# Kernel tuning notes

Hardware: AMD Instinct MI355X
Metric: run time of the kernel (lower is better)

The kernel has to match this reference:

```python
import jax, jax.numpy as jnp
import numpy as np

B, T, N = 512, 1024, 50
ROOT_IDX, END_IDX = 0, 1
NEG_INF = -10000.0


def setup_inputs() -> dict:
    key = jax.random.key(0)
    k1, k2, k3, k4 = jax.random.split(key, 4)
    input_features = jax.random.normal(k1, (B, T, N), dtype=jnp.float32)
    # xavier_uniform on [N, N]: bound = sqrt(6 / (N + N))
    bound = float(np.sqrt(6.0 / (N + N)))
    log_transitions = jax.random.uniform(k2, (N, N), minval=-bound, maxval=bound, dtype=jnp.float32)
    log_transitions = log_transitions.at[:, ROOT_IDX].set(NEG_INF)
    log_transitions = log_transitions.at[END_IDX, :].set(NEG_INF)
    target_tags = jax.random.randint(k3, (B, T), 0, N).astype(jnp.int64)
    # contiguous prefix mask from random lengths in [T//2, T]
    lengths = jax.random.randint(k4, (B,), T // 2, T + 1)
    input_mask = (jnp.arange(T)[None, :] < lengths[:, None]).astype(jnp.int32)
    return {
        "input_features": input_features,
        "log_transitions": log_transitions,
        "target_tags": target_tags,
        "input_mask": input_mask,
    }


def _crf_nll(input_features, log_transitions, target_tags, input_mask):
    maskf = input_mask.astype(input_features.dtype)  # [B, T]

    # ---- forward belief propagation (log partition) ----
    alpha0 = log_transitions[ROOT_IDX, :][None, :] + input_features[:, 0, :]  # [B, N]
    feats_t = jnp.swapaxes(input_features, 0, 1)  # [T, B, N]
    mask_t = jnp.swapaxes(maskf, 0, 1)            # [T, B]

    def step(alpha, xs):
        feat, m = xs  # [B, N], [B]
        # next_tag_var[b, i, j] = alpha[b, i] + feat[b, j] + trans[i, j]
        nxt = alpha[:, :, None] + feat[:, None, :] + log_transitions[None, :, :]
        new = jax.nn.logsumexp(nxt, axis=1)  # [B, N]
        m = m[:, None]
        return new * m + alpha * (1.0 - m), None

    alpha, _ = jax.lax.scan(step, alpha0, (feats_t[1:], mask_t[1:]))
    log_z = jax.nn.logsumexp(alpha + log_transitions[:, END_IDX][None, :], axis=-1)  # [B]

    # ---- gold sequence score (vectorized over time) ----
    tags = target_tags  # [B, T]
    scores = log_transitions[ROOT_IDX, tags[:, 0]]  # [B]
    # per-position emission score of the gold tag
    emis = jnp.take_along_axis(input_features, tags[:, :, None], axis=2)[:, :, 0]  # [B, T]
    trans = log_transitions[tags[:, :-1], tags[:, 1:]]  # [B, T-1]
    scores = scores + jnp.sum(trans * maskf[:, 1:], axis=1) + jnp.sum(emis[:, :-1] * maskf[:, :-1], axis=1)
    last_idx = jnp.sum(input_mask, axis=1) - 1  # [B]
    last_tags = jnp.take_along_axis(tags, last_idx[:, None], axis=1)[:, 0]  # [B]
    last_emit = jnp.take_along_axis(input_features[:, -1, :], last_tags[:, None], axis=1)[:, 0]
    scores = scores + log_transitions[last_tags, END_IDX] + last_emit * maskf[:, -1]

    return log_z - scores  # negative log likelihood, [B]


def reference(input_features, log_transitions, target_tags, input_mask):
    return _crf_nll(input_features, log_transitions, target_tags, input_mask)
```

## Files before the change

kernel.cpp:

```cpp
#include <hip/hip_runtime.h>
#include <math.h>

#define BB 512
#define TT 1024
#define NS 50

typedef _Float16 half2_t __attribute__((ext_vector_type(2)));

static __device__ __forceinline__ half2_t pk_h2(float a, float b) {
    auto r = __builtin_amdgcn_cvt_pkrtz(a, b);
    return __builtin_bit_cast(half2_t, r);
}
static __device__ __forceinline__ float wave_sum_f(float v) {
    #pragma unroll
    for (int k = 32; k >= 1; k >>= 1) v += __shfl_xor(v, k, 64);
    return v;
}
static __device__ __forceinline__ int wave_sum_i(int v) {
    #pragma unroll
    for (int k = 32; k >= 1; k >>= 1) v += __shfl_xor(v, k, 64);
    return v;
}
#define FDOT(a, b, c) __builtin_amdgcn_fdot2((a), (b), (c), false)

__global__ __launch_bounds__(128, 1) void crf_nll_kernel(
    const float* __restrict__ feat,
    const float* __restrict__ trans,
    const int*   __restrict__ tags,
    const int*   __restrict__ mask,
    float* __restrict__ out)
{
    const int b    = blockIdx.x;
    const int tid  = threadIdx.x;
    const int w    = tid >> 6;
    const int lane = tid & 63;
    const int jj   = (lane < NS) ? lane : 0;

    __shared__ float sh_comb[64];
    __shared__ float sh_sc[2];
    __shared__ int   sh_Kb;

#define INIT_E(m) half2_t e##m; { \
        int r0 = w ? (jj * NS + 2*(m)) : ((2*(m)) * NS + jj); \
        int r1 = r0 + (w ? 1 : NS); \
        float x0 = __expf(trans[r0]); \
        float x1 = __expf(trans[r1]); \
        if (lane >= NS) { x0 = 0.f; x1 = 0.f; } \
        e##m = pk_h2(x0, x1); }
    INIT_E(0)  INIT_E(1)  INIT_E(2)  INIT_E(3)  INIT_E(4)
    INIT_E(5)  INIT_E(6)  INIT_E(7)  INIT_E(8)  INIT_E(9)
    INIT_E(10) INIT_E(11) INIT_E(12) INIT_E(13) INIT_E(14)
    INIT_E(15) INIT_E(16) INIT_E(17) INIT_E(18) INIT_E(19)
    INIT_E(20) INIT_E(21) INIT_E(22) INIT_E(23) INIT_E(24)
#undef INIT_E

    int cnt = 0;
    for (int t = lane; t < TT; t += 64) cnt += mask[b * TT + t];
    const int len = wave_sum_i(cnt);
    const int tm  = (len - 1) >> 1;
    const int nst = w ? (len - 1 - tm) : tm;

    const float* fb = feat + (size_t)b * TT * NS;

    float u;
    if (w == 0) u = (lane < NS) ? __expf(trans[jj] + fb[jj]) : 0.f;
    else        u = (lane < NS) ? __expf(trans[jj * NS + 1] + fb[(size_t)(len - 1) * NS + jj]) : 0.f;
    int K = 0, kp, rr;
    { int bb2 = __builtin_amdgcn_readlane(__float_as_int(u), 7);
      kp = ((bb2 >> 23) & 255) - 127; rr = (127 - kp) << 23; }

    auto step = [&](float eexp) {
        K += kp;
        float p = u * __int_as_float(rr);
        int pn_ = __builtin_amdgcn_update_dpp(
            __float_as_int(p), __float_as_int(p), 0xB1, 0xF, 0xF, true);
        float pnf = __int_as_float(pn_);
        half2_t pk = pk_h2(p, pnf);
        int pki = __builtin_bit_cast(int, pk);
        float s0 = 0.f, s1 = 0.f, s2 = 0.f, s3 = 0.f;
        float s4 = 0.f, s5 = 0.f, s6 = 0.f, s7 = 0.f;
#define RLF(m, acc) { int b_ = __builtin_amdgcn_readlane(pki, 2*(m)); \
        acc = FDOT(__builtin_bit_cast(half2_t, b_), e##m, acc); }
        RLF(0,  s0) RLF(1,  s1) RLF(2,  s2) RLF(3,  s3)
        RLF(4,  s4) RLF(5,  s5) RLF(6,  s6) RLF(7,  s7)
        RLF(8,  s0) RLF(9,  s1) RLF(10, s2) RLF(11, s3)
        RLF(12, s4) RLF(13, s5) RLF(14, s6) RLF(15, s7)
        RLF(16, s0) RLF(17, s1) RLF(18, s2) RLF(19, s3)
        RLF(20, s4) RLF(21, s5) RLF(22, s6) RLF(23, s7)
        RLF(24, s0)
#undef RLF
        float S = ((s0 + s1) + (s2 + s3)) + ((s4 + s5) + (s6 + s7));
        u = S * eexp;
        int bb2 = __builtin_amdgcn_readlane(__float_as_int(u), 7);
        kp = ((bb2 >> 23) & 255) - 127;
        rr = (127 - kp) << 23;
    };

    float q0, q1, q2, q3, q4, q5, q6, q7;
    {
        int t0 = w ? (len - 2) : 1;
        int st = w ? -1 : 1;
#define LD(qr, d) { int tl = t0 + st * (d); tl = (tl < 0) ? 0 : ((tl < TT) ? tl : TT - 1); \
                    qr = __expf(fb[(size_t)tl * NS + jj]); }
        LD(q0, 0) LD(q1, 1) LD(q2, 2) LD(q3, 3) LD(q4, 4) LD(q5, 5) LD(q6, 6) LD(q7, 7)
#undef LD
    }

#define PF_STEP(qr, d) { \
        float e_ = qr; \
        int kl = k + 8 + (d); \
        int tl = w ? (len - 2 - kl) : (1 + kl); \
        tl = (tl < 0) ? 0 : ((tl < TT) ? tl : TT - 1); \
        qr = __expf(fb[(size_t)tl * NS + jj]); \
        step(e_); }

    int k = 0;
    for (; k + 8 <= nst; k += 8) {
        PF_STEP(q0, 0) PF_STEP(q1, 1) PF_STEP(q2, 2) PF_STEP(q3, 3)
        PF_STEP(q4, 4) PF_STEP(q5, 5) PF_STEP(q6, 6) PF_STEP(q7, 7)
    }
#undef PF_STEP
    for (; k < nst; ++k) {
        int tl = w ? (len - 2 - k) : (1 + k);
        step(__expf(fb[(size_t)tl * NS + jj]));
    }

    if (w == 1) {
        sh_comb[lane] = u * __expf(-fb[(size_t)tm * NS + jj]);
        if (lane == 0) sh_Kb = K;
    }

    const int* tb = tags + (size_t)b * TT;
    float sc = 0.0f;
    for (int t2 = tid; t2 < len; t2 += 128) {
        int tg = tb[t2];
        sc += fb[(size_t)t2 * NS + tg];
        if (t2 >= 1) sc += trans[tb[t2 - 1] * NS + tg];
    }
    sc = wave_sum_f(sc);
    if (lane == 0) sh_sc[w] = sc;

    __syncthreads();

    if (w == 0) {
        float wv = u * sh_comb[lane];
        float W = wave_sum_f(wv);
        float log_z = __logf(W) + (float)(K + sh_Kb) * 0.6931471805599453f;
        if (lane == 0) {
            float sct = sh_sc[0] + sh_sc[1]
                      + trans[tb[0]]
                      + trans[tb[len - 1] * NS + 1];
            out[b] = log_z - sct;
        }
    }
}

extern "C" void kernel_launch(void* const* d_in, const int* in_sizes, int n_in,
                              void* d_out, int out_size, void* d_ws, size_t ws_size,
                              hipStream_t stream) {
    const float* feat  = (const float*)d_in[0];
    const float* trans = (const float*)d_in[1];
    const int*   tags  = (const int*)d_in[2];
    const int*   mask  = (const int*)d_in[3];
    float* out = (float*)d_out;
    crf_nll_kernel<<<dim3(BB), dim3(128), 0, stream>>>(feat, trans, tags, mask, out);
}
```

Baseline: 275.3 us.

## Stage emission chunks through double-buffered LDS with coalesced float2 loads

Replaces the per-step strided global loads of emission features, previously prefetched eight steps ahead in registers, with coalesced float2 loads of 32-timestep chunks. Each chunk is exponentiated and transposed into a padded, double-buffered LDS tile, and the recurrence reads its next eight values from LDS. The aim is to take the global load latency and per-step exp off the serial dependency chain. In exchange it adds LDS traffic, index arithmetic and lgkmcnt waits, plus more complex tail handling that could contain indexing bugs.

```diff
diff --git a/kernel.cpp b/kernel.cpp
--- a/kernel.cpp
+++ b/kernel.cpp
@@ -4,6 +4,7 @@
 #define BB 512
 #define TT 1024
 #define NS 50
+#define LCOLS 33
 
 typedef _Float16 half2_t __attribute__((ext_vector_type(2)));
 
@@ -39,6 +40,7 @@
     __shared__ float sh_comb[64];
     __shared__ float sh_sc[2];
     __shared__ int   sh_Kb;
+    __shared__ float lds[2][2][NS * LCOLS];
 
 #define INIT_E(m) half2_t e##m; { \
         int r0 = w ? (jj * NS + 2*(m)) : ((2*(m)) * NS + jj); \
@@ -96,33 +98,99 @@
         rr = (127 - kp) << 23;
     };
 
-    float q0, q1, q2, q3, q4, q5, q6, q7;
-    {
-        int t0 = w ? (len - 2) : 1;
-        int st = w ? -1 : 1;
-#define LD(qr, d) { int tl = t0 + st * (d); tl = (tl < 0) ? 0 : ((tl < TT) ? tl : TT - 1); \
-                    qr = __expf(fb[(size_t)tl * NS + jj]); }
-        LD(q0, 0) LD(q1, 1) LD(q2, 2) LD(q3, 3) LD(q4, 4) LD(q5, 5) LD(q6, 6) LD(q7, 7)
-#undef LD
-    }
-
-#define PF_STEP(qr, d) { \
-        float e_ = qr; \
-        int kl = k + 8 + (d); \
-        int tl = w ? (len - 2 - kl) : (1 + kl); \
-        tl = (tl < 0) ? 0 : ((tl < TT) ? tl : TT - 1); \
-        qr = __expf(fb[(size_t)tl * NS + jj]); \
-        step(e_); }
-
-    int k = 0;
-    for (; k + 8 <= nst; k += 8) {
-        PF_STEP(q0, 0) PF_STEP(q1, 1) PF_STEP(q2, 2) PF_STEP(q3, 3)
-        PF_STEP(q4, 4) PF_STEP(q5, 5) PF_STEP(q6, 6) PF_STEP(q7, 7)
-    }
-#undef PF_STEP
-    for (; k < nst; ++k) {
-        int tl = w ? (len - 2 - k) : (1 + k);
-        step(__expf(fb[(size_t)tl * NS + jj]));
+    auto chunk_base = [&](int cs) -> int {
+        int bs = w ? (len - 33 - 32 * cs) : (1 + 32 * cs);
+        return bs < 0 ? 0 : bs;
+    };
+
+    float2 g0, g1, g2, g3, g4, g5, g6, g7, g8, g9, g10, g11, g12;
+    g12.x = 0.f; g12.y = 0.f;
+    auto issue_loads = [&](int cs) {
+        int base = chunk_base(cs);
+        const float2* gp = (const float2*)(fb + (size_t)base * NS);
+        g0  = gp[0*64  + lane];  g1  = gp[1*64  + lane];
+        g2  = gp[2*64  + lane];  g3  = gp[3*64  + lane];
+        g4  = gp[4*64  + lane];  g5  = gp[5*64  + lane];
+        g6  = gp[6*64  + lane];  g7  = gp[7*64  + lane];
+        g8  = gp[8*64  + lane];  g9  = gp[9*64  + lane];
+        g10 = gp[10*64 + lane];  g11 = gp[11*64 + lane];
+        if (lane < 32) g12 = gp[12*64 + lane];
+    };
+    auto exp_write = [&](int cs, float* L) {
+        int base = chunk_base(cs);
+        int LD2  = len - 2 - 32 * cs;
+#define WR(gi, i) { \
+        int d   = (i) * 128 + lane * 2; \
+        int r   = d / 50; \
+        int col = d - r * 50; \
+        int sr  = w ? (LD2 - (base + r)) : r; \
+        bool ok = (((i) < 12) || (lane < 32)) && (sr >= 0) && (sr < 32); \
+        if (ok) { L[col * LCOLS + sr]       = __expf(gi.x); \
+                  L[(col + 1) * LCOLS + sr] = __expf(gi.y); } }
+        WR(g0,0)  WR(g1,1)  WR(g2,2)  WR(g3,3)  WR(g4,4)  WR(g5,5)
+        WR(g6,6)  WR(g7,7)  WR(g8,8)  WR(g9,9)  WR(g10,10) WR(g11,11)
+        WR(g12,12)
+#undef WR
+    };
+
+    float c0, c1, c2, c3, c4, c5, c6, c7;
+    auto prime = [&](const float* L) {
+        const float* Lp = L + jj * LCOLS;
+        c0 = Lp[0]; c1 = Lp[1]; c2 = Lp[2]; c3 = Lp[3];
+        c4 = Lp[4]; c5 = Lp[5]; c6 = Lp[6]; c7 = Lp[7];
+    };
+
+    const int nfull = nst >> 5;
+    const int tail  = nst & 31;
+
+    issue_loads(0);
+    exp_write(0, &lds[w][0][0]);
+    issue_loads(1);
+    __asm__ volatile("s_waitcnt lgkmcnt(0)" ::: "memory");
+    __builtin_amdgcn_sched_barrier(0);
+    prime(&lds[w][0][0]);
+
+    int bufc = 0;
+    for (int c = 0; c < nfull; ++c) {
+        const float* L  = &lds[w][bufc][0] + jj * LCOLS;
+        #pragma unroll 1
+        for (int it = 0; it < 4; ++it) {
+            int nidx = ((it + 1) * 8) & 31;
+            float n0 = L[nidx + 0], n1 = L[nidx + 1], n2 = L[nidx + 2], n3 = L[nidx + 3];
+            float n4 = L[nidx + 4], n5 = L[nidx + 5], n6 = L[nidx + 6], n7 = L[nidx + 7];
+            step(c0); step(c1); step(c2); step(c3);
+            step(c4); step(c5); step(c6); step(c7);
+            c0 = n0; c1 = n1; c2 = n2; c3 = n3;
+            c4 = n4; c5 = n5; c6 = n6; c7 = n7;
+        }
+        float* Lnxt = &lds[w][bufc ^ 1][0];
+        exp_write(c + 1, Lnxt);
+        issue_loads(c + 2);
+        __asm__ volatile("s_waitcnt lgkmcnt(0)" ::: "memory");
+        __builtin_amdgcn_sched_barrier(0);
+        prime(Lnxt);
+        bufc ^= 1;
+    }
+
+    if (tail) {
+        const float* L = &lds[w][bufc][0] + jj * LCOLS;
+        int rem = tail;
+        #pragma unroll 1
+        for (int it = 0; it < 4 && rem > 0; ++it) {
+            int nidx = ((it + 1) * 8) & 31;
+            float n0 = L[nidx + 0], n1 = L[nidx + 1], n2 = L[nidx + 2], n3 = L[nidx + 3];
+            float n4 = L[nidx + 4], n5 = L[nidx + 5], n6 = L[nidx + 6], n7 = L[nidx + 7];
+            if (rem > 0) { step(c0); --rem; }
+            if (rem > 0) { step(c1); --rem; }
+            if (rem > 0) { step(c2); --rem; }
+            if (rem > 0) { step(c3); --rem; }
+            if (rem > 0) { step(c4); --rem; }
+            if (rem > 0) { step(c5); --rem; }
+            if (rem > 0) { step(c6); --rem; }
+            if (rem > 0) { step(c7); --rem; }
+            c0 = n0; c1 = n1; c2 = n2; c3 = n3;
+            c4 = n4; c5 = n5; c6 = n6; c7 = n7;
+        }
     }
 
     if (w == 1) {
```

New measurement: 288.5 us. +4.8%, slower.
